# Optimization experiments

Hardware: AMD Instinct MI355X
Metric: run time of the kernel (lower is better)

Reference implementation:

```python
import jax, jax.numpy as jnp
import numpy as np


def setup_inputs() -> dict:
    key = jax.random.key(0)
    ks = jax.random.split(key, 7)
    B, C, H, W = 8, 512, 32, 32
    N = 4
    Cn = C // N
    return {
        "first": jax.random.normal(ks[0], (B, C, H, W), dtype=jnp.float32),
        "second": jax.random.normal(ks[1], (B, C, H, W), dtype=jnp.float32),
        "w1": jax.random.normal(ks[2], (Cn, Cn), dtype=jnp.float32) * 0.05,
        "w2": jax.random.normal(ks[3], (Cn, Cn), dtype=jnp.float32) * 0.05,
        "w3": jax.random.normal(ks[4], (Cn, Cn), dtype=jnp.float32) * 0.05,
        "w4": jax.random.normal(ks[5], (Cn, Cn), dtype=jnp.float32) * 0.05,
        "w5": jax.random.normal(ks[6], (C, N), dtype=jnp.float32) * 0.05,
        "head_count": N,
    }


def reference(first, second, w1, w2, w3, w4, w5, head_count):
    B, C, H, W = first.shape
    N = head_count
    Cn = C // N
    L = H * W
    f = first.reshape(B * N, Cn, L)   # [BN, Cn, L]
    s = second.reshape(B * N, Cn, L)
    # 1x1 convs (no bias) == channel matmuls
    key_t = jnp.einsum('oc,bcl->blo', w1, f)    # [BN, L, Cn]
    query = jnp.einsum('oc,bcl->bol', w2, s)    # [BN, Cn, L]
    scores = jnp.einsum('blc,bcm->blm', key_t, query)  # [BN, L, L]
    attn = jax.nn.softmax(scores, axis=2)
    v1_t = jnp.einsum('oc,bcl->blo', w3, f)     # [BN, L, Cn]
    v2 = jnp.einsum('oc,bcl->bol', w4, s)       # [BN, Cn, L]
    value = jnp.einsum('blc,bcm->blm', v1_t, v2)  # [BN, L, L]
    res = jnp.sum(attn * value, axis=2)         # [BN, L]
    res = res.reshape(B, N, H, W)
    out = jax.nn.relu(jnp.einsum('on,bnhw->bohw', w5, res))  # [B, C, H, W]
    return out
```

## Files before the change

### kernel.cpp

```cpp
#include <hip/hip_runtime.h>
#include <hip/hip_bf16.h>
#include <stdint.h>

constexpr int BN = 32;
constexpr int Cn = 128;
constexpr int L  = 1024;
constexpr int CC = 512;
constexpr int BB = 8;

typedef __bf16 bf16x8 __attribute__((ext_vector_type(8)));
typedef float  f32x4  __attribute__((ext_vector_type(4)));
typedef unsigned short u16x8 __attribute__((ext_vector_type(8)));

__device__ inline unsigned short f2bf(float f) {
    unsigned int x = __float_as_uint(f);
    x += 0x7fffu + ((x >> 16) & 1u);
    return (unsigned short)(x >> 16);
}

__device__ inline void gl_lds16(const void* g, void* l) {
    typedef __attribute__((address_space(1))) const unsigned int GU;
    typedef __attribute__((address_space(3))) unsigned int LU;
    __builtin_amdgcn_global_load_lds((GU*)g, (LU*)l, 16, 0, 0);
}

__global__ __launch_bounds__(256)
void mkM_kernel(const float* __restrict__ w1, const float* __restrict__ w2,
                const float* __restrict__ w3, const float* __restrict__ w4,
                unsigned short* __restrict__ Mh, unsigned short* __restrict__ Ml)
{
    const int mb  = blockIdx.x;
    const int mat = mb >> 3;
    const int cq  = mb & 7;
    const int t   = threadIdx.x;
    const float* wa = mat ? w3 : w1;
    const float* wb = mat ? w4 : w2;
    const int c   = cq * 16 + (t & 15);
    const int cg2 = t >> 4;
    float acc[8];
    #pragma unroll
    for (int j = 0; j < 8; ++j) acc[j] = 0.f;
    for (int o = 0; o < 128; ++o) {
        float a = wa[o * 128 + c];
        #pragma unroll
        for (int j = 0; j < 8; ++j)
            acc[j] += a * wb[o * 128 + cg2 * 8 + j];
    }
    u16x8 hi, lo;
    #pragma unroll
    for (int j = 0; j < 8; ++j) {
        unsigned short h = f2bf(acc[j]);
        hi[j] = h;
        lo[j] = f2bf(acc[j] - __uint_as_float((unsigned)h << 16));
    }
    const int off = mat * 16384 + c * 128 + cg2 * 8;
    *(u16x8*)&Mh[off] = hi;
    *(u16x8*)&Ml[off] = lo;
}

__global__ __launch_bounds__(512, 4)
void prep_kernel(const float* __restrict__ second,
                 const unsigned short* __restrict__ Mh,
                 const unsigned short* __restrict__ Ml,
                 unsigned short* __restrict__ Y1, unsigned short* __restrict__ Y2)
{
    __shared__ unsigned short shs[64 * 128];
    __shared__ unsigned short sls[64 * 128];

    const int p  = blockIdx.x;
    const int mt = p & 15;
    const int bn = p >> 4;

    const float* s = second + (size_t)bn * Cn * L + mt * 64;

    const int tid  = threadIdx.x;
    const int lane = tid & 63;
    const int wid  = tid >> 6;
    const int mat  = wid & 1;
    const int cq   = wid >> 1;
    const int r16  = lane & 15;
    const int g    = lane >> 4;

    const unsigned short* MHm = Mh + mat * 16384;
    const unsigned short* MLm = Ml + mat * 16384;
    unsigned short* Y = (mat ? Y2 : Y1) + (size_t)bn * (L * Cn);

    bf16x8 mh[2][4], ml[2][4];
    #pragma unroll
    for (int og = 0; og < 2; ++og)
        #pragma unroll
        for (int kk = 0; kk < 4; ++kk) {
            int c  = cq * 32 + og * 16 + r16;
            int cp = kk * 32 + g * 8;
            mh[og][kk] = *(const bf16x8*)&MHm[c * 128 + cp];
            ml[og][kk] = *(const bf16x8*)&MLm[c * 128 + cp];
        }

    {
        const int sm   = tid & 63;
        const int cblk = tid >> 6;
        #pragma unroll
        for (int h = 0; h < 2; ++h) {
            const int chunk = cblk * 2 + h;
            const int c0 = chunk * 8;
            float v[8];
            #pragma unroll
            for (int j = 0; j < 8; ++j)
                v[j] = s[(size_t)(c0 + j) * L + sm];
            u16x8 hi, lo;
            #pragma unroll
            for (int j = 0; j < 8; ++j) {
                unsigned short hh = f2bf(v[j]);
                hi[j] = hh;
                lo[j] = f2bf(v[j] - __uint_as_float((unsigned)hh << 16));
            }
            const int off = sm * 128 + (chunk ^ (sm & 15)) * 8;
            *(u16x8*)&shs[off] = hi;
            *(u16x8*)&sls[off] = lo;
        }
    }
    __syncthreads();

    #pragma unroll
    for (int ms = 0; ms < 4; ++ms) {
        const int row = ms * 16 + r16;
        bf16x8 bh[4], bl[4];
        #pragma unroll
        for (int kk = 0; kk < 4; ++kk) {
            const int slot = ((kk << 2) + g) ^ r16;
            bh[kk] = *(const bf16x8*)&shs[row * 128 + slot * 8];
            bl[kk] = *(const bf16x8*)&sls[row * 128 + slot * 8];
        }
        f32x4 acc[2];
        acc[0] = (f32x4){0.f, 0.f, 0.f, 0.f};
        acc[1] = (f32x4){0.f, 0.f, 0.f, 0.f};
        #pragma unroll
        for (int kk = 0; kk < 4; ++kk)
            #pragma unroll
            for (int og = 0; og < 2; ++og) {
                f32x4 a = acc[og];
                a = __builtin_amdgcn_mfma_f32_16x16x32_bf16(mh[og][kk], bh[kk], a, 0, 0, 0);
                a = __builtin_amdgcn_mfma_f32_16x16x32_bf16(ml[og][kk], bh[kk], a, 0, 0, 0);
                a = __builtin_amdgcn_mfma_f32_16x16x32_bf16(mh[og][kk], bl[kk], a, 0, 0, 0);
                acc[og] = a;
            }
        const int m = mt * 64 + ms * 16 + r16;
        #pragma unroll
        for (int og = 0; og < 2; ++og) {
            const int c0 = cq * 32 + og * 16 + g * 4;
            f32x4 a = acc[og];
            ushort4 st;
            st.x = f2bf(a.x); st.y = f2bf(a.y);
            st.z = f2bf(a.z); st.w = f2bf(a.w);
            const int pos = (((c0 >> 3) ^ (m & 7)) << 3) | (c0 & 7);
            *(ushort4*)&Y[(size_t)m * 128 + pos] = st;
        }
    }
}

__global__ __launch_bounds__(256, 2)
void attn_kernel(const float* __restrict__ first,
                 const unsigned short* __restrict__ Y1,
                 const unsigned short* __restrict__ Y2,
                 float* __restrict__ Dp, float* __restrict__ Rp)
{
    __shared__ unsigned short fs[64 * 128];
    __shared__ char smem[2][2][16384];

    const int p   = blockIdx.x;
    const int xcd = p & 7;
    const int jj  = p >> 3;
    const int bn  = xcd * 4 + (jj & 3);
    const int lt  = (jj >> 2) & 15;
    const int mh  = jj >> 6;

    const int tid  = threadIdx.x;
    const int lane = tid & 63;
    const int w    = tid >> 6;
    const int r16  = lane & 15;
    const int g    = lane >> 4;
    const int swz  = lane & 7;

    const size_t slab = (size_t)L * Cn;
    const float* f = first + (size_t)bn * slab;
    const unsigned short* Q = Y1 + (size_t)bn * slab;
    const unsigned short* V = Y2 + (size_t)bn * slab;

    auto STAGE = [&](int buf, int t) {
        const int m0 = mh * 512 + t * 64;
        const char* qs = (const char*)Q + (size_t)m0 * 256;
        const char* vs = (const char*)V + (size_t)m0 * 256;
        char* qd = &smem[buf][0][0];
        char* vd = &smem[buf][1][0];
        #pragma unroll
        for (int it = 0; it < 4; ++it) {
            gl_lds16(qs + tid * 16 + it * 4096, qd + tid * 16 + it * 4096);
            gl_lds16(vs + tid * 16 + it * 4096, vd + tid * 16 + it * 4096);
        }
    };

    STAGE(0, 0);
    {
        const int sl   = tid & 63;
        const int cblk = tid >> 6;
        #pragma unroll
        for (int i = 0; i < 4; ++i) {
            const int chunk = cblk * 4 + i;
            const int c0 = chunk * 8;
            float v[8];
            #pragma unroll
            for (int j = 0; j < 8; ++j)
                v[j] = f[(size_t)(c0 + j) * L + lt * 64 + sl];
            u16x8 hi;
            #pragma unroll
            for (int j = 0; j < 8; ++j) hi[j] = f2bf(v[j]);
            *(u16x8*)&fs[sl * 128 + (chunk ^ (sl & 15)) * 8] = hi;
        }
    }
    __syncthreads();

    bf16x8 bf[4];
    #pragma unroll
    for (int kk = 0; kk < 4; ++kk) {
        const int row = w * 16 + r16;
        const int slot = ((kk << 2) + g) ^ r16;
        bf[kk] = *(const bf16x8*)&fs[row * 128 + slot * 8];
    }

    float Dacc = 0.f, Racc = 0.f;
    const f32x4 z = {0.f, 0.f, 0.f, 0.f};

    auto COMPUTE = [&](int buf) {
        const char* qb = &smem[buf][0][0];
        const char* vb = &smem[buf][1][0];
        #pragma unroll
        for (int mg = 0; mg < 4; ++mg) {
            const int brow = mg * 16 + r16;
            const int rbase = brow * 256;
            bf16x8 qf[4], vf[4];
            #pragma unroll
            for (int kk = 0; kk < 4; ++kk) {
                int off = rbase + ((((kk << 2) + g) ^ swz) << 4);
                qf[kk] = *(const bf16x8*)(qb + off);
                vf[kk] = *(const bf16x8*)(vb + off);
            }
            f32x4 s0 = z, u0 = z;
            #pragma unroll
            for (int kk = 0; kk < 4; ++kk) {
                s0 = __builtin_amdgcn_mfma_f32_16x16x32_bf16(qf[kk], bf[kk], s0, 0, 0, 0);
                u0 = __builtin_amdgcn_mfma_f32_16x16x32_bf16(vf[kk], bf[kk], u0, 0, 0, 0);
            }
            float e0 = __expf(s0.x - 8.f);
            float e1 = __expf(s0.y - 8.f);
            float e2 = __expf(s0.z - 8.f);
            float e3 = __expf(s0.w - 8.f);
            Dacc += (e0 + e1) + (e2 + e3);
            Racc += (e0 * u0.x + e1 * u0.y) + (e2 * u0.z + e3 * u0.w);
        }
    };

    for (int t = 0; t < 8; ++t) {
        if (t < 7) STAGE((t + 1) & 1, t + 1);
        COMPUTE(t & 1);
        __syncthreads();
    }

    Dacc += __shfl_xor(Dacc, 16);
    Racc += __shfl_xor(Racc, 16);
    Dacc += __shfl_xor(Dacc, 32);
    Racc += __shfl_xor(Racc, 32);

    if (g == 0) {
        const int l = lt * 64 + w * 16 + r16;
        size_t idx = (size_t)mh * BN * L + (size_t)bn * L + l;
        Dp[idx] = Dacc;
        Rp[idx] = Racc;
    }
}

__global__ __launch_bounds__(256)
void combine_kernel(const float* __restrict__ Dp, const float* __restrict__ Rp,
                    float* __restrict__ res)
{
    int i = blockIdx.x * 256 + threadIdx.x;
    float d = Dp[i] + Dp[BN * L + i];
    float r = Rp[i] + Rp[BN * L + i];
    res[i] = r / d;
}

__global__ __launch_bounds__(256)
void out_kernel(const float* __restrict__ res, const float* __restrict__ w5,
                float* __restrict__ out)
{
    const int blk = blockIdx.x;
    const int o = blk & 511;
    const int b = blk >> 9;
    const float4 wv = *(const float4*)&w5[o * 4];

    const float* r0 = res + (size_t)(b * 4 + 0) * L;
    const float* r1 = res + (size_t)(b * 4 + 1) * L;
    const float* r2 = res + (size_t)(b * 4 + 2) * L;
    const float* r3 = res + (size_t)(b * 4 + 3) * L;

    const int hw = threadIdx.x * 4;
    float4 a0 = *(const float4*)&r0[hw];
    float4 a1 = *(const float4*)&r1[hw];
    float4 a2 = *(const float4*)&r2[hw];
    float4 a3 = *(const float4*)&r3[hw];

    float4 ov;
    ov.x = fmaxf(0.f, wv.x * a0.x + wv.y * a1.x + wv.z * a2.x + wv.w * a3.x);
    ov.y = fmaxf(0.f, wv.x * a0.y + wv.y * a1.y + wv.z * a2.y + wv.w * a3.y);
    ov.z = fmaxf(0.f, wv.x * a0.z + wv.y * a1.z + wv.z * a2.z + wv.w * a3.z);
    ov.w = fmaxf(0.f, wv.x * a0.w + wv.y * a1.w + wv.z * a2.w + wv.w * a3.w);

    *(float4*)&out[(size_t)blk * 1024 + hw] = ov;
}

extern "C" void kernel_launch(void* const* d_in, const int* in_sizes, int n_in,
                              void* d_out, int out_size, void* d_ws, size_t ws_size,
                              hipStream_t stream)
{
    const float* first  = (const float*)d_in[0];
    const float* second = (const float*)d_in[1];
    const float* w1 = (const float*)d_in[2];
    const float* w2 = (const float*)d_in[3];
    const float* w3 = (const float*)d_in[4];
    const float* w4 = (const float*)d_in[5];
    const float* w5 = (const float*)d_in[6];
    float* out = (float*)d_out;

    const size_t slabElems = (size_t)L * Cn;
    const size_t arr = (size_t)BN * slabElems;

    unsigned short* Y1 = (unsigned short*)d_ws;
    unsigned short* Y2 = Y1 + arr;
    unsigned short* Mh = Y2 + arr;
    unsigned short* Ml = Mh + 2 * 16384;
    float* Dp  = (float*)(Ml + 2 * 16384);
    float* Rp  = Dp + 2 * BN * L;
    float* res = Rp + 2 * BN * L;

    mkM_kernel<<<dim3(16), dim3(256), 0, stream>>>(w1, w2, w3, w4, Mh, Ml);
    prep_kernel<<<dim3(512), dim3(512), 0, stream>>>(second, Mh, Ml, Y1, Y2);
    attn_kernel<<<dim3(1024), dim3(256), 0, stream>>>(first, Y1, Y2, Dp, Rp);
    combine_kernel<<<dim3(BN * L / 256), dim3(256), 0, stream>>>(Dp, Rp, res);
    out_kernel<<<dim3(BB * CC), dim3(256), 0, stream>>>(res, w5, out);
}
```

Baseline: 70.04 us.

## Drop m-split in attention, fuse combine, and stage prep output through LDS

The attention kernel no longer splits the key dimension across two blocks. Each block now loops over all 16 m-tiles and writes the normalized result directly, which removes the combine kernel and the partial D/R buffers. The prep kernel now assembles its Y tiles in shared memory and writes them out with coalesced 16-byte stores instead of scattered 8-byte stores. The trade-off is a grid halved to 512 attention blocks, which lowers parallelism on a large GPU and doubles the serial loop length per block. The prep kernel also uses 32KB more LDS, which may reduce its occupancy.

New measurement: 71.28 us. Within noise of the previous version (+1.8%).

```diff
diff --git a/kernel.cpp b/kernel.cpp
--- a/kernel.cpp
+++ b/kernel.cpp
@@ -66,6 +66,7 @@
 {
     __shared__ unsigned short shs[64 * 128];
     __shared__ unsigned short sls[64 * 128];
+    __shared__ unsigned short yrep[2][64 * 128];
 
     const int p  = blockIdx.x;
     const int mt = p & 15;
@@ -83,7 +84,6 @@
 
     const unsigned short* MHm = Mh + mat * 16384;
     const unsigned short* MLm = Ml + mat * 16384;
-    unsigned short* Y = (mat ? Y2 : Y1) + (size_t)bn * (L * Cn);
 
     bf16x8 mh[2][4], ml[2][4];
     #pragma unroll
@@ -144,7 +144,7 @@
                 a = __builtin_amdgcn_mfma_f32_16x16x32_bf16(mh[og][kk], bl[kk], a, 0, 0, 0);
                 acc[og] = a;
             }
-        const int m = mt * 64 + ms * 16 + r16;
+        const int m = ms * 16 + r16;
         #pragma unroll
         for (int og = 0; og < 2; ++og) {
             const int c0 = cq * 32 + og * 16 + g * 4;
@@ -153,7 +153,19 @@
             st.x = f2bf(a.x); st.y = f2bf(a.y);
             st.z = f2bf(a.z); st.w = f2bf(a.w);
             const int pos = (((c0 >> 3) ^ (m & 7)) << 3) | (c0 & 7);
-            *(ushort4*)&Y[(size_t)m * 128 + pos] = st;
+            *(ushort4*)&yrep[mat][m * 128 + pos] = st;
+        }
+    }
+    __syncthreads();
+
+    {
+        unsigned short* Y1t = Y1 + (size_t)bn * (L * Cn) + mt * 8192;
+        unsigned short* Y2t = Y2 + (size_t)bn * (L * Cn) + mt * 8192;
+        #pragma unroll
+        for (int i = 0; i < 2; ++i) {
+            const int off = (i * 512 + tid) * 8;
+            *(u16x8*)&Y1t[off] = *(const u16x8*)&yrep[0][off];
+            *(u16x8*)&Y2t[off] = *(const u16x8*)&yrep[1][off];
         }
     }
 }
@@ -162,7 +174,7 @@
 void attn_kernel(const float* __restrict__ first,
                  const unsigned short* __restrict__ Y1,
                  const unsigned short* __restrict__ Y2,
-                 float* __restrict__ Dp, float* __restrict__ Rp)
+                 float* __restrict__ res)
 {
     __shared__ unsigned short fs[64 * 128];
     __shared__ char smem[2][2][16384];
@@ -171,8 +183,7 @@
     const int xcd = p & 7;
     const int jj  = p >> 3;
     const int bn  = xcd * 4 + (jj & 3);
-    const int lt  = (jj >> 2) & 15;
-    const int mh  = jj >> 6;
+    const int lt  = jj >> 2;
 
     const int tid  = threadIdx.x;
     const int lane = tid & 63;
@@ -187,7 +198,7 @@
     const unsigned short* V = Y2 + (size_t)bn * slab;
 
     auto STAGE = [&](int buf, int t) {
-        const int m0 = mh * 512 + t * 64;
+        const int m0 = t * 64;
         const char* qs = (const char*)Q + (size_t)m0 * 256;
         const char* vs = (const char*)V + (size_t)m0 * 256;
         char* qd = &smem[buf][0][0];
@@ -259,8 +270,8 @@
         }
     };
 
-    for (int t = 0; t < 8; ++t) {
-        if (t < 7) STAGE((t + 1) & 1, t + 1);
+    for (int t = 0; t < 16; ++t) {
+        if (t < 15) STAGE((t + 1) & 1, t + 1);
         COMPUTE(t & 1);
         __syncthreads();
     }
@@ -272,20 +283,8 @@
 
     if (g == 0) {
         const int l = lt * 64 + w * 16 + r16;
-        size_t idx = (size_t)mh * BN * L + (size_t)bn * L + l;
-        Dp[idx] = Dacc;
-        Rp[idx] = Racc;
-    }
-}
-
-__global__ __launch_bounds__(256)
-void combine_kernel(const float* __restrict__ Dp, const float* __restrict__ Rp,
-                    float* __restrict__ res)
-{
-    int i = blockIdx.x * 256 + threadIdx.x;
-    float d = Dp[i] + Dp[BN * L + i];
-    float r = Rp[i] + Rp[BN * L + i];
-    res[i] = r / d;
+        res[(size_t)bn * L + l] = Racc / Dacc;
+    }
 }
 
 __global__ __launch_bounds__(256)
@@ -337,13 +336,10 @@
     unsigned short* Y2 = Y1 + arr;
     unsigned short* Mh = Y2 + arr;
     unsigned short* Ml = Mh + 2 * 16384;
-    float* Dp  = (float*)(Ml + 2 * 16384);
-    float* Rp  = Dp + 2 * BN * L;
-    float* res = Rp + 2 * BN * L;
+    float* res = (float*)(Ml + 2 * 16384);
 
     mkM_kernel<<<dim3(16), dim3(256), 0, stream>>>(w1, w2, w3, w4, Mh, Ml);
     prep_kernel<<<dim3(512), dim3(512), 0, stream>>>(second, Mh, Ml, Y1, Y2);
-    attn_kernel<<<dim3(1024), dim3(256), 0, stream>>>(first, Y1, Y2, Dp, Rp);
-    combine_kernel<<<dim3(BN * L / 256), dim3(256), 0, stream>>>(Dp, Rp, res);
+    attn_kernel<<<dim3(512), dim3(256), 0, stream>>>(first, Y1, Y2, res);
     out_kernel<<<dim3(BB * CC), dim3(256), 0, stream>>>(res, w5, out);
 }
```
